# Performance work log

Measured on AMD Instinct MI355X. Metric: run time of the kernel, lower is better.

Reference implementation:

```python
import jax, jax.numpy as jnp
import numpy as np

CE_W, DICE_W, BD_W = 1.0, 3.0, 2.0   # combined-loss lambdas
BPW = 10.0                            # boundary pixel weight
SMOOTH = 1e-6                         # dice smoothing
# cv2.getStructuringElement(cv2.MORPH_ELLIPSE, (5,5))
ELLIPSE5 = np.array([[0,0,1,0,0],
                     [1,1,1,1,1],
                     [1,1,1,1,1],
                     [1,1,1,1,1],
                     [0,0,1,0,0]], dtype=bool)


def setup_inputs() -> dict:
    key = jax.random.key(0)
    k1, k2 = jax.random.split(key)
    B, C, H, W = 8, 8, 512, 1024
    pred = jax.random.normal(k1, (B, C, H, W), dtype=jnp.float32)
    target = jax.random.randint(k2, (B, H, W), 0, C).astype(jnp.int32)
    return {"pred": pred, "target": target}


def _morph(mask, is_dilate):
    """Grayscale dilate/erode with 5x5 ellipse SE (matches cv2 default border:
    padding value never wins the max/min)."""
    pad_val = 0 if is_dilate else jnp.iinfo(jnp.int32).max
    p = jnp.pad(mask, ((0, 0), (2, 2), (2, 2)), constant_values=pad_val)
    H, W = mask.shape[1], mask.shape[2]
    out = None
    for dy in range(5):
        for dx in range(5):
            if not ELLIPSE5[dy, dx]:
                continue
            s = p[:, dy:dy + H, dx:dx + W]
            if out is None:
                out = s
            else:
                out = jnp.maximum(out, s) if is_dilate else jnp.minimum(out, s)
    return out


def reference(pred, target):
    B, C, H, W = pred.shape
    logp = jax.nn.log_softmax(pred, axis=1)                         # (B,C,H,W)
    # per-pixel cross entropy
    ce_map = -jnp.take_along_axis(logp, target[:, None], axis=1)[:, 0]  # (B,H,W)
    ce = ce_map.mean()
    # dice over softmax probs vs one-hot target
    probs = jnp.exp(logp)
    onehot = jax.nn.one_hot(target, C, dtype=pred.dtype, axis=1)    # (B,C,H,W)
    inter = jnp.sum(probs * onehot, axis=(2, 3))                    # (B,C)
    card = jnp.sum(probs, axis=(2, 3)) + jnp.sum(onehot, axis=(2, 3))
    dice = 1.0 - jnp.mean((2.0 * inter + SMOOTH) / (card + SMOOTH))
    # boundary mask = morphological gradient of the label map
    t = target.astype(jnp.int32)
    boundary = _morph(t, True) - _morph(t, False)                   # (B,H,W)
    wmap = jnp.where(boundary > 0, jnp.float32(BPW), jnp.float32(1.0))
    bd = jnp.mean(ce_map * wmap)
    return CE_W * ce + DICE_W * dice + BD_W * bd
```

## Files before the change

### kernel.cpp

```cpp
#include <hip/hip_runtime.h>
#include <math.h>

constexpr int B = 8, C = 8, H = 512, W = 1024;
constexpr int RH = 2;
constexpr int NT = 256;
constexpr float BPW = 10.0f;
constexpr float SMOOTH = 1e-6f;

constexpr int ACC_N = 2 + 3 * B * C;

__device__ __forceinline__ unsigned win_or5(unsigned lo, unsigned mid, unsigned hi) {
    unsigned long long a = ((unsigned long long)mid << 32) | lo;
    unsigned long long b = ((unsigned long long)hi << 32) | mid;
    return (unsigned)(a >> 16) | (unsigned)(a >> 24) | mid |
           (unsigned)(b >> 8) | (unsigned)(b >> 16);
}

__device__ __forceinline__ unsigned pack_row(const int* __restrict__ tb, int gh, int gc) {
    if (gh < 0 || gh >= H || gc < 0 || gc >= W) return 0u;
    const int4 t4 = *reinterpret_cast<const int4*>(tb + (size_t)gh * W + gc);
    return (1u << t4.x) | ((1u << t4.y) << 8) | ((1u << t4.z) << 16) | ((1u << t4.w) << 24);
}

__global__ __launch_bounds__(NT)
void loss_main(const float* __restrict__ pred, const int* __restrict__ target,
               float* __restrict__ acc) {
    __shared__ float sred[4][26];

    const int tid = threadIdx.x;
    const int h0 = blockIdx.x * RH;
    const int b  = blockIdx.y;
    const int gc = tid * 4;

    const int* tb = target + (size_t)b * H * W;
    const size_t plane = (size_t)H * W;
    const float* pb = pred + (size_t)b * C * plane + (size_t)h0 * W + gc;

    const unsigned c0 = pack_row(tb, h0 - 2, gc);
    const unsigned c1 = pack_row(tb, h0 - 1, gc);
    const unsigned c2 = pack_row(tb, h0,     gc);
    const unsigned c3 = pack_row(tb, h0 + 1, gc);
    const unsigned c4 = pack_row(tb, h0 + 2, gc);
    const unsigned c5 = pack_row(tb, h0 + 3, gc);
    const unsigned l0 = pack_row(tb, h0 - 1, gc - 4);
    const unsigned l1 = pack_row(tb, h0,     gc - 4);
    const unsigned l2 = pack_row(tb, h0 + 1, gc - 4);
    const unsigned l3 = pack_row(tb, h0 + 2, gc - 4);
    const unsigned r0 = pack_row(tb, h0 - 1, gc + 4);
    const unsigned r1 = pack_row(tb, h0,     gc + 4);
    const unsigned r2 = pack_row(tb, h0 + 1, gc + 4);
    const unsigned r3 = pack_row(tb, h0 + 2, gc + 4);

    float4 xa[C], xb[C];
#pragma unroll
    for (int c = 0; c < C; ++c) xa[c] = *reinterpret_cast<const float4*>(pb + c * plane);
#pragma unroll
    for (int c = 0; c < C; ++c) xb[c] = *reinterpret_cast<const float4*>(pb + c * plane + W);

    float ce_s = 0.f, bd_s = 0.f;
    float p_s[C], in_s[C];
    unsigned cnt = 0u;
#pragma unroll
    for (int c = 0; c < C; ++c) { p_s[c] = 0.f; in_s[c] = 0.f; }

    const unsigned bmA = win_or5(l0 | l1 | l2, c1 | c2 | c3, r0 | r1 | r2) | c0 | c4;
    const unsigned bmB = win_or5(l1 | l2 | l3, c2 | c3 | c4, r1 | r2 | r3) | c1 | c5;

#pragma unroll
    for (int s = 0; s < 2; ++s) {
        const float4* x = (s == 0) ? xa : xb;
        const unsigned cmid = (s == 0) ? c2 : c3;
        const unsigned bm4  = (s == 0) ? bmA : bmB;

#pragma unroll
        for (int j = 0; j < 4; ++j) {
            const float x0 = (j==0)?x[0].x:(j==1)?x[0].y:(j==2)?x[0].z:x[0].w;
            const float x1 = (j==0)?x[1].x:(j==1)?x[1].y:(j==2)?x[1].z:x[1].w;
            const float x2 = (j==0)?x[2].x:(j==1)?x[2].y:(j==2)?x[2].z:x[2].w;
            const float x3 = (j==0)?x[3].x:(j==1)?x[3].y:(j==2)?x[3].z:x[3].w;
            const float x4 = (j==0)?x[4].x:(j==1)?x[4].y:(j==2)?x[4].z:x[4].w;
            const float x5 = (j==0)?x[5].x:(j==1)?x[5].y:(j==2)?x[5].z:x[5].w;
            const float x6 = (j==0)?x[6].x:(j==1)?x[6].y:(j==2)?x[6].z:x[6].w;
            const float x7 = (j==0)?x[7].x:(j==1)?x[7].y:(j==2)?x[7].z:x[7].w;

            const float e0 = __expf(x0), e1 = __expf(x1), e2 = __expf(x2), e3 = __expf(x3);
            const float e4 = __expf(x4), e5 = __expf(x5), e6 = __expf(x6), e7 = __expf(x7);
            const float sum = ((e0 + e1) + (e2 + e3)) + ((e4 + e5) + (e6 + e7));
            const float invs = __builtin_amdgcn_rcpf(sum);

            const unsigned cm  = (cmid >> (8 * j)) & 0xFFu;
            const unsigned bmj = (bm4  >> (8 * j)) & 0xFFu;
            const int t = 31 - __clz(cm);

            const float p0 = e0 * invs, p1 = e1 * invs, p2 = e2 * invs, p3 = e3 * invs;
            const float p4 = e4 * invs, p5 = e5 * invs, p6 = e6 * invs, p7 = e7 * invs;
            p_s[0] += p0; p_s[1] += p1; p_s[2] += p2; p_s[3] += p3;
            p_s[4] += p4; p_s[5] += p5; p_s[6] += p6; p_s[7] += p7;

            const bool b0 = (t == 0), b1 = (t == 1), b2 = (t == 2), b3 = (t == 3);
            const bool b4 = (t == 4), b5 = (t == 5), b6 = (t == 6), b7 = (t == 7);
            in_s[0] += b0 ? p0 : 0.f;  in_s[1] += b1 ? p1 : 0.f;
            in_s[2] += b2 ? p2 : 0.f;  in_s[3] += b3 ? p3 : 0.f;
            in_s[4] += b4 ? p4 : 0.f;  in_s[5] += b5 ? p5 : 0.f;
            in_s[6] += b6 ? p6 : 0.f;  in_s[7] += b7 ? p7 : 0.f;

            float pt = p0;
            pt = b1 ? p1 : pt;  pt = b2 ? p2 : pt;  pt = b3 ? p3 : pt;
            pt = b4 ? p4 : pt;  pt = b5 ? p5 : pt;  pt = b6 ? p6 : pt;
            pt = b7 ? p7 : pt;
            const float l = __logf(pt);
            const float wgt = (bmj & (bmj - 1u)) ? BPW : 1.f;
            ce_s -= l;
            bd_s = fmaf(-l, wgt, bd_s);
            cnt += 1u << (t << 2);
        }
    }

    float vals[26];
    vals[0] = ce_s; vals[1] = bd_s;
#pragma unroll
    for (int c = 0; c < C; ++c) {
        vals[2 + c]  = p_s[c];
        vals[10 + c] = in_s[c];
        vals[18 + c] = (float)((cnt >> (4 * c)) & 0xFu);
    }
#pragma unroll
    for (int k = 0; k < 26; ++k) {
        float v = vals[k];
#pragma unroll
        for (int off = 32; off > 0; off >>= 1) v += __shfl_down(v, off, 64);
        vals[k] = v;
    }
    const int lane = tid & 63, wid = tid >> 6;
    if (lane == 0) {
#pragma unroll
        for (int k = 0; k < 26; ++k) sred[wid][k] = vals[k];
    }
    __syncthreads();
    if (tid < 26) {
        const float v = sred[0][tid] + sred[1][tid] + sred[2][tid] + sred[3][tid];
        int gi;
        if (tid == 0)       gi = 0;
        else if (tid == 1)  gi = 1;
        else if (tid < 10)  gi = 2 + b * C + (tid - 2);
        else if (tid < 18)  gi = 2 + B * C + b * C + (tid - 10);
        else                gi = 2 + 2 * B * C + b * C + (tid - 18);
        atomicAdd(&acc[gi], v);
    }
}

__global__ void loss_final(const float* __restrict__ acc, float* __restrict__ out) {
    const int i = threadIdx.x;
    const float psum  = acc[2 + i];
    const float inter = acc[2 + B * C + i];
    const float cnt   = acc[2 + 2 * B * C + i];
    float d = (2.f * inter + SMOOTH) / (psum + cnt + SMOOTH);
#pragma unroll
    for (int off = 32; off > 0; off >>= 1) d += __shfl_down(d, off, 64);
    if (i == 0) {
        const float N = (float)B * H * W;
        const float ce = acc[0] / N;
        const float bd = acc[1] / N;
        const float dice = 1.f - d / (float)(B * C);
        out[0] = 1.0f * ce + 3.0f * dice + 2.0f * bd;
    }
}

extern "C" void kernel_launch(void* const* d_in, const int* in_sizes, int n_in,
                              void* d_out, int out_size, void* d_ws, size_t ws_size,
                              hipStream_t stream) {
    const float* pred = (const float*)d_in[0];
    const int* target = (const int*)d_in[1];
    float* acc = (float*)d_ws;
    float* out = (float*)d_out;

    hipMemsetAsync(acc, 0, ACC_N * sizeof(float), stream);

    dim3 grid(H / RH, B);
    loss_main<<<grid, NT, 0, stream>>>(pred, target, acc);
    loss_final<<<1, 64, 0, stream>>>(acc, out);
}
```

Measured before the change: 211.1 us.

## Split boundary/label prep into a separate kernel writing packed per-pixel info bytes

Moves the morphological boundary computation and label counting into a prep kernel that writes one byte per pixel (class id plus a boundary flag) to workspace. The main kernel then reads this compact byte map instead of gathering 14 int4 target rows with halo, and processes one row per block with fewer live registers. The aim is to cut the redundant halo loads of target and the register pressure in the pred-streaming kernel. The cost is an extra launch plus an 8 MB write and read of the info buffer.

New measurement: 258.4 us. 22.4% more time.

```diff
diff --git a/kernel.cpp b/kernel.cpp
--- a/kernel.cpp
+++ b/kernel.cpp
@@ -2,11 +2,11 @@
 #include <math.h>
 
 constexpr int B = 8, C = 8, H = 512, W = 1024;
-constexpr int RH = 2;
 constexpr int NT = 256;
 constexpr float BPW = 10.0f;
 constexpr float SMOOTH = 1e-6f;
 
+constexpr size_t INFO_BYTES = (size_t)B * H * W;
 constexpr int ACC_N = 2 + 3 * B * C;
 
 __device__ __forceinline__ unsigned win_or5(unsigned lo, unsigned mid, unsigned hi) {
@@ -22,19 +22,30 @@
     return (1u << t4.x) | ((1u << t4.y) << 8) | ((1u << t4.z) << 16) | ((1u << t4.w) << 24);
 }
 
+__device__ __forceinline__ unsigned info4(unsigned cmid, unsigned bm4) {
+    unsigned out = 0u;
+#pragma unroll
+    for (int j = 0; j < 4; ++j) {
+        const unsigned cm  = (cmid >> (8 * j)) & 0xFFu;
+        const unsigned bmj = (bm4  >> (8 * j)) & 0xFFu;
+        const unsigned t   = 31u - __clz(cm);
+        const unsigned bd  = (bmj & (bmj - 1u)) ? 8u : 0u;
+        out |= (t | bd) << (8 * j);
+    }
+    return out;
+}
+
 __global__ __launch_bounds__(NT)
-void loss_main(const float* __restrict__ pred, const int* __restrict__ target,
-               float* __restrict__ acc) {
-    __shared__ float sred[4][26];
+void prep(const int* __restrict__ target, unsigned* __restrict__ info,
+          float* __restrict__ acc) {
+    __shared__ float sred[4][8];
 
     const int tid = threadIdx.x;
-    const int h0 = blockIdx.x * RH;
+    const int h0 = blockIdx.x * 2;
     const int b  = blockIdx.y;
     const int gc = tid * 4;
 
     const int* tb = target + (size_t)b * H * W;
-    const size_t plane = (size_t)H * W;
-    const float* pb = pred + (size_t)b * C * plane + (size_t)h0 * W + gc;
 
     const unsigned c0 = pack_row(tb, h0 - 2, gc);
     const unsigned c1 = pack_row(tb, h0 - 1, gc);
@@ -51,81 +62,114 @@
     const unsigned r2 = pack_row(tb, h0 + 1, gc + 4);
     const unsigned r3 = pack_row(tb, h0 + 2, gc + 4);
 
-    float4 xa[C], xb[C];
-#pragma unroll
-    for (int c = 0; c < C; ++c) xa[c] = *reinterpret_cast<const float4*>(pb + c * plane);
-#pragma unroll
-    for (int c = 0; c < C; ++c) xb[c] = *reinterpret_cast<const float4*>(pb + c * plane + W);
+    const unsigned bmA = win_or5(l0 | l1 | l2, c1 | c2 | c3, r0 | r1 | r2) | c0 | c4;
+    const unsigned bmB = win_or5(l1 | l2 | l3, c2 | c3 | c4, r1 | r2 | r3) | c1 | c5;
+
+    const unsigned iA = info4(c2, bmA);
+    const unsigned iB = info4(c3, bmB);
+    const size_t base = ((size_t)b * H + h0) * W + gc;
+    info[base >> 2]       = iA;
+    info[(base + W) >> 2] = iB;
+
+    unsigned cnt = 0u;
+#pragma unroll
+    for (int j = 0; j < 4; ++j) {
+        cnt += 1u << (((iA >> (8 * j)) & 7u) << 2);
+        cnt += 1u << (((iB >> (8 * j)) & 7u) << 2);
+    }
+    float vals[8];
+#pragma unroll
+    for (int c = 0; c < C; ++c) vals[c] = (float)((cnt >> (4 * c)) & 0xFu);
+#pragma unroll
+    for (int k = 0; k < 8; ++k) {
+        float v = vals[k];
+#pragma unroll
+        for (int off = 32; off > 0; off >>= 1) v += __shfl_down(v, off, 64);
+        vals[k] = v;
+    }
+    const int lane = tid & 63, wid = tid >> 6;
+    if (lane == 0) {
+#pragma unroll
+        for (int k = 0; k < 8; ++k) sred[wid][k] = vals[k];
+    }
+    __syncthreads();
+    if (tid < 8) {
+        const float v = sred[0][tid] + sred[1][tid] + sred[2][tid] + sred[3][tid];
+        atomicAdd(&acc[2 + 2 * B * C + b * C + tid], v);
+    }
+}
+
+__global__ __launch_bounds__(NT)
+void loss_main(const float* __restrict__ pred, const unsigned* __restrict__ info,
+               float* __restrict__ acc) {
+    __shared__ float sred[4][18];
+
+    const int tid = threadIdx.x;
+    const int h = blockIdx.x;
+    const int b = blockIdx.y;
+    const int gc = tid * 4;
+
+    const size_t plane = (size_t)H * W;
+    const size_t base = ((size_t)b * H + h) * W + gc;
+    const float* pp = pred + (size_t)b * C * plane + (size_t)h * W + gc;
+
+    const unsigned inf = info[base >> 2];
+    float4 x[C];
+#pragma unroll
+    for (int c = 0; c < C; ++c) x[c] = *reinterpret_cast<const float4*>(pp + c * plane);
 
     float ce_s = 0.f, bd_s = 0.f;
     float p_s[C], in_s[C];
-    unsigned cnt = 0u;
 #pragma unroll
     for (int c = 0; c < C; ++c) { p_s[c] = 0.f; in_s[c] = 0.f; }
 
-    const unsigned bmA = win_or5(l0 | l1 | l2, c1 | c2 | c3, r0 | r1 | r2) | c0 | c4;
-    const unsigned bmB = win_or5(l1 | l2 | l3, c2 | c3 | c4, r1 | r2 | r3) | c1 | c5;
-
-#pragma unroll
-    for (int s = 0; s < 2; ++s) {
-        const float4* x = (s == 0) ? xa : xb;
-        const unsigned cmid = (s == 0) ? c2 : c3;
-        const unsigned bm4  = (s == 0) ? bmA : bmB;
-
-#pragma unroll
-        for (int j = 0; j < 4; ++j) {
-            const float x0 = (j==0)?x[0].x:(j==1)?x[0].y:(j==2)?x[0].z:x[0].w;
-            const float x1 = (j==0)?x[1].x:(j==1)?x[1].y:(j==2)?x[1].z:x[1].w;
-            const float x2 = (j==0)?x[2].x:(j==1)?x[2].y:(j==2)?x[2].z:x[2].w;
-            const float x3 = (j==0)?x[3].x:(j==1)?x[3].y:(j==2)?x[3].z:x[3].w;
-            const float x4 = (j==0)?x[4].x:(j==1)?x[4].y:(j==2)?x[4].z:x[4].w;
-            const float x5 = (j==0)?x[5].x:(j==1)?x[5].y:(j==2)?x[5].z:x[5].w;
-            const float x6 = (j==0)?x[6].x:(j==1)?x[6].y:(j==2)?x[6].z:x[6].w;
-            const float x7 = (j==0)?x[7].x:(j==1)?x[7].y:(j==2)?x[7].z:x[7].w;
-
-            const float e0 = __expf(x0), e1 = __expf(x1), e2 = __expf(x2), e3 = __expf(x3);
-            const float e4 = __expf(x4), e5 = __expf(x5), e6 = __expf(x6), e7 = __expf(x7);
-            const float sum = ((e0 + e1) + (e2 + e3)) + ((e4 + e5) + (e6 + e7));
-            const float invs = __builtin_amdgcn_rcpf(sum);
-
-            const unsigned cm  = (cmid >> (8 * j)) & 0xFFu;
-            const unsigned bmj = (bm4  >> (8 * j)) & 0xFFu;
-            const int t = 31 - __clz(cm);
-
-            const float p0 = e0 * invs, p1 = e1 * invs, p2 = e2 * invs, p3 = e3 * invs;
-            const float p4 = e4 * invs, p5 = e5 * invs, p6 = e6 * invs, p7 = e7 * invs;
-            p_s[0] += p0; p_s[1] += p1; p_s[2] += p2; p_s[3] += p3;
-            p_s[4] += p4; p_s[5] += p5; p_s[6] += p6; p_s[7] += p7;
-
-            const bool b0 = (t == 0), b1 = (t == 1), b2 = (t == 2), b3 = (t == 3);
-            const bool b4 = (t == 4), b5 = (t == 5), b6 = (t == 6), b7 = (t == 7);
-            in_s[0] += b0 ? p0 : 0.f;  in_s[1] += b1 ? p1 : 0.f;
-            in_s[2] += b2 ? p2 : 0.f;  in_s[3] += b3 ? p3 : 0.f;
-            in_s[4] += b4 ? p4 : 0.f;  in_s[5] += b5 ? p5 : 0.f;
-            in_s[6] += b6 ? p6 : 0.f;  in_s[7] += b7 ? p7 : 0.f;
-
-            float pt = p0;
-            pt = b1 ? p1 : pt;  pt = b2 ? p2 : pt;  pt = b3 ? p3 : pt;
-            pt = b4 ? p4 : pt;  pt = b5 ? p5 : pt;  pt = b6 ? p6 : pt;
-            pt = b7 ? p7 : pt;
-            const float l = __logf(pt);
-            const float wgt = (bmj & (bmj - 1u)) ? BPW : 1.f;
-            ce_s -= l;
-            bd_s = fmaf(-l, wgt, bd_s);
-            cnt += 1u << (t << 2);
-        }
-    }
-
-    float vals[26];
+#pragma unroll
+    for (int j = 0; j < 4; ++j) {
+        const float x0 = (j==0)?x[0].x:(j==1)?x[0].y:(j==2)?x[0].z:x[0].w;
+        const float x1 = (j==0)?x[1].x:(j==1)?x[1].y:(j==2)?x[1].z:x[1].w;
+        const float x2 = (j==0)?x[2].x:(j==1)?x[2].y:(j==2)?x[2].z:x[2].w;
+        const float x3 = (j==0)?x[3].x:(j==1)?x[3].y:(j==2)?x[3].z:x[3].w;
+        const float x4 = (j==0)?x[4].x:(j==1)?x[4].y:(j==2)?x[4].z:x[4].w;
+        const float x5 = (j==0)?x[5].x:(j==1)?x[5].y:(j==2)?x[5].z:x[5].w;
+        const float x6 = (j==0)?x[6].x:(j==1)?x[6].y:(j==2)?x[6].z:x[6].w;
+        const float x7 = (j==0)?x[7].x:(j==1)?x[7].y:(j==2)?x[7].z:x[7].w;
+
+        const float e0 = __expf(x0), e1 = __expf(x1), e2 = __expf(x2), e3 = __expf(x3);
+        const float e4 = __expf(x4), e5 = __expf(x5), e6 = __expf(x6), e7 = __expf(x7);
+        const float sum = ((e0 + e1) + (e2 + e3)) + ((e4 + e5) + (e6 + e7));
+        const float invs = __builtin_amdgcn_rcpf(sum);
+
+        const unsigned ib = (inf >> (8 * j)) & 0xFu;
+        const int t = (int)(ib & 7u);
+
+        const float p0 = e0 * invs, p1 = e1 * invs, p2 = e2 * invs, p3 = e3 * invs;
+        const float p4 = e4 * invs, p5 = e5 * invs, p6 = e6 * invs, p7 = e7 * invs;
+        p_s[0] += p0; p_s[1] += p1; p_s[2] += p2; p_s[3] += p3;
+        p_s[4] += p4; p_s[5] += p5; p_s[6] += p6; p_s[7] += p7;
+
+        const bool b0 = (t == 0), b1 = (t == 1), b2 = (t == 2), b3 = (t == 3);
+        const bool b4 = (t == 4), b5 = (t == 5), b6 = (t == 6), b7 = (t == 7);
+        in_s[0] += b0 ? p0 : 0.f;  in_s[1] += b1 ? p1 : 0.f;
+        in_s[2] += b2 ? p2 : 0.f;  in_s[3] += b3 ? p3 : 0.f;
+        in_s[4] += b4 ? p4 : 0.f;  in_s[5] += b5 ? p5 : 0.f;
+        in_s[6] += b6 ? p6 : 0.f;  in_s[7] += b7 ? p7 : 0.f;
+
+        float pt = p0;
+        pt = b1 ? p1 : pt;  pt = b2 ? p2 : pt;  pt = b3 ? p3 : pt;
+        pt = b4 ? p4 : pt;  pt = b5 ? p5 : pt;  pt = b6 ? p6 : pt;
+        pt = b7 ? p7 : pt;
+        const float l = __logf(pt);
+        const float wgt = (ib & 8u) ? BPW : 1.f;
+        ce_s -= l;
+        bd_s = fmaf(-l, wgt, bd_s);
+    }
+
+    float vals[18];
     vals[0] = ce_s; vals[1] = bd_s;
 #pragma unroll
-    for (int c = 0; c < C; ++c) {
-        vals[2 + c]  = p_s[c];
-        vals[10 + c] = in_s[c];
-        vals[18 + c] = (float)((cnt >> (4 * c)) & 0xFu);
-    }
-#pragma unroll
-    for (int k = 0; k < 26; ++k) {
+    for (int c = 0; c < C; ++c) { vals[2 + c] = p_s[c]; vals[10 + c] = in_s[c]; }
+#pragma unroll
+    for (int k = 0; k < 18; ++k) {
         float v = vals[k];
 #pragma unroll
         for (int off = 32; off > 0; off >>= 1) v += __shfl_down(v, off, 64);
@@ -134,17 +178,16 @@
     const int lane = tid & 63, wid = tid >> 6;
     if (lane == 0) {
 #pragma unroll
-        for (int k = 0; k < 26; ++k) sred[wid][k] = vals[k];
+        for (int k = 0; k < 18; ++k) sred[wid][k] = vals[k];
     }
     __syncthreads();
-    if (tid < 26) {
+    if (tid < 18) {
         const float v = sred[0][tid] + sred[1][tid] + sred[2][tid] + sred[3][tid];
         int gi;
         if (tid == 0)       gi = 0;
         else if (tid == 1)  gi = 1;
         else if (tid < 10)  gi = 2 + b * C + (tid - 2);
-        else if (tid < 18)  gi = 2 + B * C + b * C + (tid - 10);
-        else                gi = 2 + 2 * B * C + b * C + (tid - 18);
+        else                gi = 2 + B * C + b * C + (tid - 10);
         atomicAdd(&acc[gi], v);
     }
 }
@@ -171,12 +214,17 @@
                               hipStream_t stream) {
     const float* pred = (const float*)d_in[0];
     const int* target = (const int*)d_in[1];
-    float* acc = (float*)d_ws;
+    unsigned* info = (unsigned*)d_ws;
+    float* acc = (float*)((char*)d_ws + INFO_BYTES);
     float* out = (float*)d_out;
 
     hipMemsetAsync(acc, 0, ACC_N * sizeof(float), stream);
 
-    dim3 grid(H / RH, B);
-    loss_main<<<grid, NT, 0, stream>>>(pred, target, acc);
+    dim3 gprep(H / 2, B);
+    prep<<<gprep, NT, 0, stream>>>(target, info, acc);
+
+    dim3 gmain(H, B);
+    loss_main<<<gmain, NT, 0, stream>>>(pred, info, acc);
+
     loss_final<<<1, 64, 0, stream>>>(acc, out);
 }
```

## Replace global atomics with per-row partials and one row per block

Applied to the files above, without the earlier changes.

Each block now handles one row instead of two and writes its 26 reduced values to a per-(batch, value, row) partial buffer instead of issuing global atomicAdds. The memset is gone, and a 1024-thread final kernel sums the partials. The inner math is reworked: the exponentials are computed in place, the target probability is selected before scaling, and the dice intersection adds pt directly. An empty asm barrier forces all pred loads to be issued before the target loads. This removes atomic contention and the memset launch, at the cost of twice as many blocks each doing the per-block reduction, and less target-halo reuse per block.

New measurement: 224.0 us. 6.1% more time.

```diff
diff --git a/kernel.cpp b/kernel.cpp
--- a/kernel.cpp
+++ b/kernel.cpp
@@ -2,12 +2,12 @@
 #include <math.h>
 
 constexpr int B = 8, C = 8, H = 512, W = 1024;
-constexpr int RH = 2;
 constexpr int NT = 256;
+constexpr int NV = 26;
 constexpr float BPW = 10.0f;
 constexpr float SMOOTH = 1e-6f;
 
-constexpr int ACC_N = 2 + 3 * B * C;
+typedef float v4f __attribute__((ext_vector_type(4)));
 
 __device__ __forceinline__ unsigned win_or5(unsigned lo, unsigned mid, unsigned hi) {
     unsigned long long a = ((unsigned long long)mid << 32) | lo;
@@ -24,99 +24,76 @@
 
 __global__ __launch_bounds__(NT)
 void loss_main(const float* __restrict__ pred, const int* __restrict__ target,
-               float* __restrict__ acc) {
-    __shared__ float sred[4][26];
+               float* __restrict__ part) {
+    __shared__ float sred[4][NV];
 
     const int tid = threadIdx.x;
-    const int h0 = blockIdx.x * RH;
-    const int b  = blockIdx.y;
+    const int h = blockIdx.x;
+    const int b = blockIdx.y;
     const int gc = tid * 4;
 
+    const size_t plane = (size_t)H * W;
+    const float* pp = pred + (size_t)b * C * plane + (size_t)h * W + gc;
+    v4f e[C];
+#pragma unroll
+    for (int c = 0; c < C; ++c) e[c] = *reinterpret_cast<const v4f*>(pp + c * plane);
+    asm volatile("" : "+v"(e[0]), "+v"(e[1]), "+v"(e[2]), "+v"(e[3]),
+                      "+v"(e[4]), "+v"(e[5]), "+v"(e[6]), "+v"(e[7]));
+
     const int* tb = target + (size_t)b * H * W;
-    const size_t plane = (size_t)H * W;
-    const float* pb = pred + (size_t)b * C * plane + (size_t)h0 * W + gc;
+    const unsigned cm2 = pack_row(tb, h - 2, gc);
+    const unsigned cm1 = pack_row(tb, h - 1, gc);
+    const unsigned cc  = pack_row(tb, h,     gc);
+    const unsigned cp1 = pack_row(tb, h + 1, gc);
+    const unsigned cp2 = pack_row(tb, h + 2, gc);
+    const unsigned lm  = pack_row(tb, h - 1, gc - 4) | pack_row(tb, h, gc - 4)
+                       | pack_row(tb, h + 1, gc - 4);
+    const unsigned rm  = pack_row(tb, h - 1, gc + 4) | pack_row(tb, h, gc + 4)
+                       | pack_row(tb, h + 1, gc + 4);
+    const unsigned bm4 = win_or5(lm, cm1 | cc | cp1, rm) | cm2 | cp2;
 
-    const unsigned c0 = pack_row(tb, h0 - 2, gc);
-    const unsigned c1 = pack_row(tb, h0 - 1, gc);
-    const unsigned c2 = pack_row(tb, h0,     gc);
-    const unsigned c3 = pack_row(tb, h0 + 1, gc);
-    const unsigned c4 = pack_row(tb, h0 + 2, gc);
-    const unsigned c5 = pack_row(tb, h0 + 3, gc);
-    const unsigned l0 = pack_row(tb, h0 - 1, gc - 4);
-    const unsigned l1 = pack_row(tb, h0,     gc - 4);
-    const unsigned l2 = pack_row(tb, h0 + 1, gc - 4);
-    const unsigned l3 = pack_row(tb, h0 + 2, gc - 4);
-    const unsigned r0 = pack_row(tb, h0 - 1, gc + 4);
-    const unsigned r1 = pack_row(tb, h0,     gc + 4);
-    const unsigned r2 = pack_row(tb, h0 + 1, gc + 4);
-    const unsigned r3 = pack_row(tb, h0 + 2, gc + 4);
-
-    float4 xa[C], xb[C];
 #pragma unroll
-    for (int c = 0; c < C; ++c) xa[c] = *reinterpret_cast<const float4*>(pb + c * plane);
-#pragma unroll
-    for (int c = 0; c < C; ++c) xb[c] = *reinterpret_cast<const float4*>(pb + c * plane + W);
+    for (int c = 0; c < C; ++c) {
+        e[c][0] = __expf(e[c][0]); e[c][1] = __expf(e[c][1]);
+        e[c][2] = __expf(e[c][2]); e[c][3] = __expf(e[c][3]);
+    }
 
     float ce_s = 0.f, bd_s = 0.f;
-    float p_s[C], in_s[C];
+    float p_s[C] = {}, in_s[C] = {};
     unsigned cnt = 0u;
-#pragma unroll
-    for (int c = 0; c < C; ++c) { p_s[c] = 0.f; in_s[c] = 0.f; }
-
-    const unsigned bmA = win_or5(l0 | l1 | l2, c1 | c2 | c3, r0 | r1 | r2) | c0 | c4;
-    const unsigned bmB = win_or5(l1 | l2 | l3, c2 | c3 | c4, r1 | r2 | r3) | c1 | c5;
 
 #pragma unroll
-    for (int s = 0; s < 2; ++s) {
-        const float4* x = (s == 0) ? xa : xb;
-        const unsigned cmid = (s == 0) ? c2 : c3;
-        const unsigned bm4  = (s == 0) ? bmA : bmB;
+    for (int j = 0; j < 4; ++j) {
+        const float sum = ((e[0][j] + e[1][j]) + (e[2][j] + e[3][j]))
+                        + ((e[4][j] + e[5][j]) + (e[6][j] + e[7][j]));
+        const float invs = __builtin_amdgcn_rcpf(sum);
+
+        const unsigned cb = (cc  >> (8 * j)) & 0xFFu;
+        const unsigned bb = (bm4 >> (8 * j)) & 0xFFu;
+        const int t = 31 - __clz(cb);
+
+        const bool b1 = (t == 1), b2 = (t == 2), b3 = (t == 3), b4 = (t == 4),
+                   b5 = (t == 5), b6 = (t == 6), b7 = (t == 7);
+        float et = e[0][j];
+        et = b1 ? e[1][j] : et;  et = b2 ? e[2][j] : et;  et = b3 ? e[3][j] : et;
+        et = b4 ? e[4][j] : et;  et = b5 ? e[5][j] : et;  et = b6 ? e[6][j] : et;
+        et = b7 ? e[7][j] : et;
+        const float pt = et * invs;
+        const float l = __logf(pt);
+        const float wgt = (bb & (bb - 1u)) ? BPW : 1.f;
+        ce_s -= l;
+        bd_s = fmaf(-l, wgt, bd_s);
+        cnt += 1u << (t << 2);
 
 #pragma unroll
-        for (int j = 0; j < 4; ++j) {
-            const float x0 = (j==0)?x[0].x:(j==1)?x[0].y:(j==2)?x[0].z:x[0].w;
-            const float x1 = (j==0)?x[1].x:(j==1)?x[1].y:(j==2)?x[1].z:x[1].w;
-            const float x2 = (j==0)?x[2].x:(j==1)?x[2].y:(j==2)?x[2].z:x[2].w;
-            const float x3 = (j==0)?x[3].x:(j==1)?x[3].y:(j==2)?x[3].z:x[3].w;
-            const float x4 = (j==0)?x[4].x:(j==1)?x[4].y:(j==2)?x[4].z:x[4].w;
-            const float x5 = (j==0)?x[5].x:(j==1)?x[5].y:(j==2)?x[5].z:x[5].w;
-            const float x6 = (j==0)?x[6].x:(j==1)?x[6].y:(j==2)?x[6].z:x[6].w;
-            const float x7 = (j==0)?x[7].x:(j==1)?x[7].y:(j==2)?x[7].z:x[7].w;
-
-            const float e0 = __expf(x0), e1 = __expf(x1), e2 = __expf(x2), e3 = __expf(x3);
-            const float e4 = __expf(x4), e5 = __expf(x5), e6 = __expf(x6), e7 = __expf(x7);
-            const float sum = ((e0 + e1) + (e2 + e3)) + ((e4 + e5) + (e6 + e7));
-            const float invs = __builtin_amdgcn_rcpf(sum);
-
-            const unsigned cm  = (cmid >> (8 * j)) & 0xFFu;
-            const unsigned bmj = (bm4  >> (8 * j)) & 0xFFu;
-            const int t = 31 - __clz(cm);
-
-            const float p0 = e0 * invs, p1 = e1 * invs, p2 = e2 * invs, p3 = e3 * invs;
-            const float p4 = e4 * invs, p5 = e5 * invs, p6 = e6 * invs, p7 = e7 * invs;
-            p_s[0] += p0; p_s[1] += p1; p_s[2] += p2; p_s[3] += p3;
-            p_s[4] += p4; p_s[5] += p5; p_s[6] += p6; p_s[7] += p7;
-
-            const bool b0 = (t == 0), b1 = (t == 1), b2 = (t == 2), b3 = (t == 3);
-            const bool b4 = (t == 4), b5 = (t == 5), b6 = (t == 6), b7 = (t == 7);
-            in_s[0] += b0 ? p0 : 0.f;  in_s[1] += b1 ? p1 : 0.f;
-            in_s[2] += b2 ? p2 : 0.f;  in_s[3] += b3 ? p3 : 0.f;
-            in_s[4] += b4 ? p4 : 0.f;  in_s[5] += b5 ? p5 : 0.f;
-            in_s[6] += b6 ? p6 : 0.f;  in_s[7] += b7 ? p7 : 0.f;
-
-            float pt = p0;
-            pt = b1 ? p1 : pt;  pt = b2 ? p2 : pt;  pt = b3 ? p3 : pt;
-            pt = b4 ? p4 : pt;  pt = b5 ? p5 : pt;  pt = b6 ? p6 : pt;
-            pt = b7 ? p7 : pt;
-            const float l = __logf(pt);
-            const float wgt = (bmj & (bmj - 1u)) ? BPW : 1.f;
-            ce_s -= l;
-            bd_s = fmaf(-l, wgt, bd_s);
-            cnt += 1u << (t << 2);
-        }
+        for (int c = 0; c < C; ++c) p_s[c] = fmaf(e[c][j], invs, p_s[c]);
+        in_s[0] += (t == 0) ? pt : 0.f;  in_s[1] += b1 ? pt : 0.f;
+        in_s[2] += b2 ? pt : 0.f;        in_s[3] += b3 ? pt : 0.f;
+        in_s[4] += b4 ? pt : 0.f;        in_s[5] += b5 ? pt : 0.f;
+        in_s[6] += b6 ? pt : 0.f;        in_s[7] += b7 ? pt : 0.f;
     }
 
-    float vals[26];
+    float vals[NV];
     vals[0] = ce_s; vals[1] = bd_s;
 #pragma unroll
     for (int c = 0; c < C; ++c) {
@@ -125,7 +102,7 @@
         vals[18 + c] = (float)((cnt >> (4 * c)) & 0xFu);
     }
 #pragma unroll
-    for (int k = 0; k < 26; ++k) {
+    for (int k = 0; k < NV; ++k) {
         float v = vals[k];
 #pragma unroll
         for (int off = 32; off > 0; off >>= 1) v += __shfl_down(v, off, 64);
@@ -134,35 +111,50 @@
     const int lane = tid & 63, wid = tid >> 6;
     if (lane == 0) {
 #pragma unroll
-        for (int k = 0; k < 26; ++k) sred[wid][k] = vals[k];
+        for (int k = 0; k < NV; ++k) sred[wid][k] = vals[k];
     }
     __syncthreads();
-    if (tid < 26) {
+    if (tid < NV) {
         const float v = sred[0][tid] + sred[1][tid] + sred[2][tid] + sred[3][tid];
-        int gi;
-        if (tid == 0)       gi = 0;
-        else if (tid == 1)  gi = 1;
-        else if (tid < 10)  gi = 2 + b * C + (tid - 2);
-        else if (tid < 18)  gi = 2 + B * C + b * C + (tid - 10);
-        else                gi = 2 + 2 * B * C + b * C + (tid - 18);
-        atomicAdd(&acc[gi], v);
+        part[((size_t)b * NV + tid) * H + h] = v;
     }
 }
 
-__global__ void loss_final(const float* __restrict__ acc, float* __restrict__ out) {
-    const int i = threadIdx.x;
-    const float psum  = acc[2 + i];
-    const float inter = acc[2 + B * C + i];
-    const float cnt   = acc[2 + 2 * B * C + i];
-    float d = (2.f * inter + SMOOTH) / (psum + cnt + SMOOTH);
+__global__ __launch_bounds__(1024)
+void loss_final(const float* __restrict__ part, float* __restrict__ out) {
+    __shared__ float s[B * NV];
+    const int tid = threadIdx.x;
+    const int lane = tid & 63, w = tid >> 6;
+
 #pragma unroll
-    for (int off = 32; off > 0; off >>= 1) d += __shfl_down(d, off, 64);
-    if (i == 0) {
-        const float N = (float)B * H * W;
-        const float ce = acc[0] / N;
-        const float bd = acc[1] / N;
-        const float dice = 1.f - d / (float)(B * C);
-        out[0] = 1.0f * ce + 3.0f * dice + 2.0f * bd;
+    for (int i = 0; i < 13; ++i) {
+        const int pair = w * 13 + i;
+        const float* p = part + (size_t)pair * H;
+        float v = 0.f;
+#pragma unroll
+        for (int r = 0; r < H / 64; ++r) v += p[lane + 64 * r];
+#pragma unroll
+        for (int off = 32; off > 0; off >>= 1) v += __shfl_down(v, off, 64);
+        if (lane == 0) s[pair] = v;
+    }
+    __syncthreads();
+
+    if (tid < 64) {
+        const int b = tid >> 3, c = tid & 7;
+        const float psum  = s[b * NV + 2 + c];
+        const float inter = s[b * NV + 10 + c];
+        const float cn    = s[b * NV + 18 + c];
+        float d = (2.f * inter + SMOOTH) / (psum + cn + SMOOTH);
+#pragma unroll
+        for (int off = 32; off > 0; off >>= 1) d += __shfl_down(d, off, 64);
+        if (tid == 0) {
+            float ce = 0.f, bd = 0.f;
+#pragma unroll
+            for (int bb = 0; bb < B; ++bb) { ce += s[bb * NV]; bd += s[bb * NV + 1]; }
+            const float N = (float)B * H * W;
+            const float dice = 1.f - d / (float)(B * C);
+            out[0] = ce / N + 3.f * dice + 2.f * bd / N;
+        }
     }
 }
 
@@ -171,12 +163,10 @@
                               hipStream_t stream) {
     const float* pred = (const float*)d_in[0];
     const int* target = (const int*)d_in[1];
-    float* acc = (float*)d_ws;
+    float* part = (float*)d_ws;
     float* out = (float*)d_out;
 
-    hipMemsetAsync(acc, 0, ACC_N * sizeof(float), stream);
-
-    dim3 grid(H / RH, B);
-    loss_main<<<grid, NT, 0, stream>>>(pred, target, acc);
-    loss_final<<<1, 64, 0, stream>>>(acc, out);
+    dim3 gmain(H, B);
+    loss_main<<<gmain, NT, 0, stream>>>(pred, target, part);
+    loss_final<<<1, 1024, 0, stream>>>(part, out);
 }
```
